# Performance work log

Hardware: AMD Instinct MI355X
Metric: run time of the kernel (lower is better)

## Reference

```python
import jax, jax.numpy as jnp
import numpy as np

N_FILTERS = 1024
N_HEADS = 16


def setup_inputs() -> dict:
    key = jax.random.key(0)
    k1, k2, k3 = jax.random.split(key, 3)
    x = jax.random.normal(k1, (8, 1024, N_FILTERS), dtype=jnp.float32)
    # VarianceScaling(0.02) ~ small dense init; 0.02*sqrt(1/fan_in) scale approximated
    w_qkv = jax.random.normal(k2, (N_FILTERS, N_FILTERS * 3), dtype=jnp.float32) * (0.02 / N_FILTERS) ** 0.5
    w_out = jax.random.normal(k3, (N_FILTERS, N_FILTERS), dtype=jnp.float32) * (0.02 / N_FILTERS) ** 0.5
    return {"x": x, "w_qkv": w_qkv, "w_out": w_out}


def reference(x, w_qkv, w_out):
    b, n, c = x.shape
    h = N_HEADS
    d = c // h
    qkv = jnp.einsum('bnc,ce->bne', x, w_qkv)  # [b, n, 3c]
    q, k, v = jnp.split(qkv, 3, axis=-1)
    # b n (h d) -> b h n d
    to_heads = lambda t: t.reshape(b, n, h, d).transpose(0, 2, 1, 3)
    q, k, v = to_heads(q), to_heads(k), to_heads(v)
    scale = jnp.sqrt(jnp.asarray(c, jnp.float32))  # NOTE: sqrt(n_filters), matches source
    attn = jnp.einsum('bhnd,bhmd->bhnm', q, k) / scale
    attn = jax.nn.softmax(attn, axis=-1)
    out = jnp.einsum('bhnm,bhmd->bhnd', attn, v)
    out = out.transpose(0, 2, 1, 3).reshape(b, n, c)  # b h n d -> b n (h d)
    return jnp.einsum('bnc,co->bno', out, w_out)
```

## Files before the change

### kernel.cpp

```cpp
#include <hip/hip_runtime.h>
#include <hip/hip_bf16.h>

typedef __bf16 bf16_t;
typedef __bf16 bf16x8 __attribute__((ext_vector_type(8)));
typedef __bf16 bf16x4 __attribute__((ext_vector_type(4)));
typedef float f32x4 __attribute__((ext_vector_type(4)));

constexpr int LD = 3072;

#define MFMA_16x16x32(a, b, c) __builtin_amdgcn_mfma_f32_16x16x32_bf16((a), (b), (c), 0, 0, 0)

#define GLOAD_LDS16(g, l)                                               \
  __builtin_amdgcn_global_load_lds(                                     \
      (const __attribute__((address_space(1))) void*)(g),               \
      (__attribute__((address_space(3))) void*)(l), 16, 0, 0)

#define TRREAD(dst, addr, imm) \
  asm volatile("ds_read_b64_tr_b16 %0, %1 offset:" imm : "=v"(dst) : "v"(addr))

#define BAR __builtin_amdgcn_s_barrier()
#define LGKM0 do { asm volatile("s_waitcnt lgkmcnt(0)" ::: "memory"); \
                   __builtin_amdgcn_sched_barrier(0); } while (0)

__global__ __launch_bounds__(256) void prep_kernel(
    const float* __restrict__ x, bf16_t* __restrict__ x_b,
    const float* __restrict__ w_qkv, bf16_t* __restrict__ wqT,
    const float* __restrict__ w_out, bf16_t* __restrict__ woT) {
  const int blk = blockIdx.x;
  if (blk < 4096) {
    const int i = blk * 256 + threadIdx.x;
    const float4 a = reinterpret_cast<const float4*>(x)[2 * i];
    const float4 c = reinterpret_cast<const float4*>(x)[2 * i + 1];
    bf16x8 o;
    o[0] = (bf16_t)a.x; o[1] = (bf16_t)a.y; o[2] = (bf16_t)a.z; o[3] = (bf16_t)a.w;
    o[4] = (bf16_t)c.x; o[5] = (bf16_t)c.y; o[6] = (bf16_t)c.z; o[7] = (bf16_t)c.w;
    reinterpret_cast<bf16x8*>(x_b)[i] = o;
    return;
  }
  __shared__ float tile[32][33];
  const float* in; bf16_t* outp; int C, bx, by;
  if (blk < 7168) { const int i = blk - 4096; in = w_qkv; outp = wqT; C = 3072; bx = i % 96; by = i / 96; }
  else            { const int i = blk - 7168; in = w_out; outp = woT; C = 1024; bx = i & 31; by = i >> 5; }
  constexpr int R = 1024;
  const int c0 = bx * 32, r0 = by * 32;
  const int tx = threadIdx.x & 31, ty = threadIdx.x >> 5;
#pragma unroll
  for (int i = 0; i < 32; i += 8)
    tile[ty + i][tx] = in[(size_t)(r0 + ty + i) * C + (c0 + tx)];
  __syncthreads();
#pragma unroll
  for (int i = 0; i < 32; i += 8)
    outp[(size_t)(c0 + ty + i) * R + (r0 + tx)] = (bf16_t)tile[tx][ty + i];
}

__global__ __launch_bounds__(512, 2) void gemm_qkv_256(
    const bf16_t* __restrict__ A, const bf16_t* __restrict__ Bt,
    bf16_t* __restrict__ C, float q_scale) {
  constexpr int K = 1024;
  extern __shared__ char smem[];
  char* asB = smem;
  char* bsB = smem + 65536;

  const int t = threadIdx.x;
  const int lane = t & 63, wave = t >> 6;
  const int l15 = lane & 15, lg = lane >> 4;
  const int wr = wave >> 2, wc = wave & 3;

  const int bid = blockIdx.x;
  const int wg = (bid & 7) * 48 + (bid >> 3);
  const int brow = (wg & 31) * 256;
  const int bcol = (wg >> 5) * 256;

  const int srow = t >> 3;
  const int schk = (t & 7) ^ (srow & 7);
  const bf16_t* aS = A + (size_t)(brow + srow) * K + schk * 8;
  const bf16_t* bS = Bt + (size_t)(bcol + srow) * K + schk * 8;
  const int ldst = t * 8;

#define STG_A(T, H) do {                                                      \
    const bf16_t* _s = aS + (size_t)((H) * 128) * K + (T) * 64;               \
    bf16_t* _d = (bf16_t*)(asB + ((T) & 1) * 32768 + (H) * 16384) + ldst;     \
    GLOAD_LDS16(_s, _d);                                                      \
    GLOAD_LDS16(_s + (size_t)64 * K, _d + 4096);                              \
  } while (0)
#define STG_B(T, H) do {                                                      \
    const bf16_t* _s = bS + (size_t)((H) * 128) * K + (T) * 64;               \
    bf16_t* _d = (bf16_t*)(bsB + ((T) & 1) * 32768 + (H) * 16384) + ldst;     \
    GLOAD_LDS16(_s, _d);                                                      \
    GLOAD_LDS16(_s + (size_t)64 * K, _d + 4096);                              \
  } while (0)

  const int rx = l15 & 7;
  const unsigned c0 = ((unsigned)(lg ^ rx)) << 4;
  const unsigned c1 = ((unsigned)((4 | lg) ^ rx)) << 4;
  const unsigned a_rd = (unsigned)(wr * 16384 + l15 * 128);
  const unsigned b_rd = (unsigned)((wc >> 1) * 16384 + (wc & 1) * 8192 + l15 * 128);

  f32x4 acc[8][4] = {};
  bf16x8 af[4][2], bfr[2][2];

#define RD_AF(BUF, MH) do { _Pragma("unroll")                                 \
    for (int m = 0; m < 4; ++m) {                                             \
      const char* _p = asB + (BUF) * 32768 + a_rd + ((MH) * 4 + m) * 2048;    \
      af[m][0] = *(const bf16x8*)(_p + c0);                                   \
      af[m][1] = *(const bf16x8*)(_p + c1); } } while (0)
#define RD_BF(BUF, NH) do { _Pragma("unroll")                                 \
    for (int n = 0; n < 2; ++n) {                                             \
      const char* _p = bsB + (BUF) * 32768 + b_rd + ((NH) * 2 + n) * 2048;    \
      bfr[n][0] = *(const bf16x8*)(_p + c0);                                  \
      bfr[n][1] = *(const bf16x8*)(_p + c1); } } while (0)
#define MM16(MH, NH) do {                                                     \
    __builtin_amdgcn_s_setprio(1);                                            \
    _Pragma("unroll")                                                         \
    for (int m = 0; m < 4; ++m) { _Pragma("unroll")                           \
      for (int n = 0; n < 2; ++n) {                                           \
        acc[(MH)*4+m][(NH)*2+n] =                                             \
            MFMA_16x16x32(af[m][0], bfr[n][0], acc[(MH)*4+m][(NH)*2+n]);      \
        acc[(MH)*4+m][(NH)*2+n] =                                             \
            MFMA_16x16x32(af[m][1], bfr[n][1], acc[(MH)*4+m][(NH)*2+n]); } }  \
    __builtin_amdgcn_s_setprio(0); } while (0)

  STG_A(0, 0); STG_A(0, 1); STG_B(0, 0); STG_B(0, 1); STG_A(1, 0);
  asm volatile("s_waitcnt vmcnt(2)" ::: "memory");
  BAR;

  for (int i = 0; i < 8; ++i) {
    const int T1 = 2 * i + 1, T2 = 2 * i + 2, T3 = 2 * i + 3;
    const bool pf = (i < 7);
    STG_A(T1, 1);
    RD_AF(0, 0); RD_BF(0, 0);
    BAR; LGKM0; MM16(0, 0); BAR;
    STG_B(T1, 0);
    RD_BF(0, 1);
    BAR; LGKM0; MM16(0, 1); BAR;
    STG_B(T1, 1);
    RD_AF(0, 1);
    BAR; LGKM0; MM16(1, 1); BAR;
    if (pf) STG_A(T2, 0);
    RD_BF(0, 0);
    BAR; LGKM0; MM16(1, 0);
    if (pf) asm volatile("s_waitcnt vmcnt(2)" ::: "memory");
    else    asm volatile("s_waitcnt vmcnt(0)" ::: "memory");
    BAR;
    if (pf) STG_A(T2, 1);
    RD_AF(1, 0); RD_BF(1, 0);
    BAR; LGKM0; MM16(0, 0); BAR;
    if (pf) STG_B(T2, 0);
    RD_BF(1, 1);
    BAR; LGKM0; MM16(0, 1); BAR;
    if (pf) STG_B(T2, 1);
    RD_AF(1, 1);
    BAR; LGKM0; MM16(1, 1); BAR;
    if (pf) STG_A(T3, 0);
    RD_BF(1, 0);
    BAR; LGKM0; MM16(1, 0);
    asm volatile("s_waitcnt vmcnt(2)" ::: "memory");
    BAR;
  }

  const float sc = (bcol < 1024) ? q_scale : 1.0f;
  const int crow0 = brow + wr * 128 + lg * 4;
  const int ccol0 = bcol + wc * 64 + l15;
#pragma unroll
  for (int m = 0; m < 8; ++m)
#pragma unroll
    for (int n = 0; n < 4; ++n)
#pragma unroll
      for (int r = 0; r < 4; ++r)
        C[(size_t)(crow0 + m * 16 + r) * 3072 + ccol0 + n * 16] =
            (bf16_t)(acc[m][n][r] * sc);
#undef STG_A
#undef STG_B
#undef RD_AF
#undef RD_BF
#undef MM16
}

template <typename OutT>
__global__ __launch_bounds__(512, 1) void gemm_bt_128x256(
    const bf16_t* __restrict__ A, const bf16_t* __restrict__ Bt,
    OutT* __restrict__ C, int N, int nrowblk, int q_cols, float q_scale) {
  constexpr int K = 1024;
  extern __shared__ char smem[];
  char* asB = smem;
  char* bsB = smem + 49152;

  const int t = threadIdx.x;
  const int lane = t & 63, wave = t >> 6;
  const int l15 = lane & 15, lg = lane >> 4;
  const int wr = wave >> 2, wc = wave & 3;

  const int cpx = (int)gridDim.x >> 3;
  const int bid = blockIdx.x;
  const int wg = (bid & 7) * cpx + (bid >> 3);
  const int brow = (wg % nrowblk) * 128;
  const int bcol = (wg / nrowblk) * 256;

  const int srow = t >> 3;
  const int schk = (t & 7) ^ (srow & 7);
  const bf16_t* aS = A + (size_t)(brow + srow) * K + schk * 8;
  const bf16_t* bS = Bt + (size_t)(bcol + srow) * K + schk * 8;
  const int ldst = t * 8;

#define STG_A(T, BUF) do {                                               \
    const bf16_t* _s = aS + (T) * 64;                                    \
    bf16_t* _d = (bf16_t*)(asB + (BUF) * 16384) + ldst;                  \
    GLOAD_LDS16(_s, _d);                                                 \
    GLOAD_LDS16(_s + (size_t)64 * K, _d + 4096);                         \
  } while (0)
#define STG_B(T, H, BUF) do {                                            \
    const bf16_t* _s = bS + (size_t)((H) * 128) * K + (T) * 64;          \
    bf16_t* _d = (bf16_t*)(bsB + (BUF) * 32768 + (H) * 16384) + ldst;    \
    GLOAD_LDS16(_s, _d);                                                 \
    GLOAD_LDS16(_s + (size_t)64 * K, _d + 4096);                         \
  } while (0)

  const int rx = l15 & 7;
  const unsigned c0 = ((unsigned)(lg ^ rx)) << 4;
  const unsigned c1 = ((unsigned)((4 | lg) ^ rx)) << 4;
  const unsigned a_rd = (unsigned)(wr * 8192 + l15 * 128);
  const unsigned b_rd = (unsigned)((wc >> 1) * 16384 + (wc & 1) * 8192 + l15 * 128);

  f32x4 acc[4][4] = {};
  bf16x8 af[2][2], bfr[4][2];

#define RD_AF(BUF, MH) do { _Pragma("unroll")                            \
    for (int m = 0; m < 2; ++m) {                                        \
      const char* _p = asB + (BUF) * 16384 + a_rd + ((MH) * 2 + m) * 2048; \
      af[m][0] = *(const bf16x8*)(_p + c0);                              \
      af[m][1] = *(const bf16x8*)(_p + c1); } } while (0)
#define RD_BF(BUF) do { _Pragma("unroll")                                \
    for (int n = 0; n < 4; ++n) {                                        \
      const char* _p = bsB + (BUF) * 32768 + b_rd + n * 2048;            \
      bfr[n][0] = *(const bf16x8*)(_p + c0);                             \
      bfr[n][1] = *(const bf16x8*)(_p + c1); } } while (0)
#define MM(MH) do {                                                      \
    __builtin_amdgcn_s_setprio(1);                                       \
    _Pragma("unroll")                                                    \
    for (int m = 0; m < 2; ++m) { _Pragma("unroll")                      \
      for (int n = 0; n < 4; ++n) {                                      \
        acc[(MH)*2+m][n] =                                               \
            MFMA_16x16x32(af[m][0], bfr[n][0], acc[(MH)*2+m][n]);        \
        acc[(MH)*2+m][n] =                                               \
            MFMA_16x16x32(af[m][1], bfr[n][1], acc[(MH)*2+m][n]); } }    \
    __builtin_amdgcn_s_setprio(0); } while (0)

  STG_A(0, 0); STG_B(0, 0, 0); STG_B(0, 1, 0);
  STG_A(1, 1); STG_B(1, 0, 1); STG_B(1, 1, 1);
  asm volatile("s_waitcnt vmcnt(6)" ::: "memory");
  BAR;

  int bc = 0;
  for (int T = 0; T < 16; ++T) {
    const bool pf = (T + 2 < 16);
    const int bs = (bc >= 1) ? (bc - 1) : 2;
    if (pf) { STG_A(T + 2, bs); STG_B(T + 2, 0, bs); }
    RD_AF(bc, 0);
    RD_BF(bc);
    BAR; LGKM0; MM(0); BAR;
    if (pf) STG_B(T + 2, 1, bs);
    RD_AF(bc, 1);
    BAR; LGKM0; MM(1);
    if (pf) asm volatile("s_waitcnt vmcnt(6)" ::: "memory");
    else    asm volatile("s_waitcnt vmcnt(0)" ::: "memory");
    BAR;
    bc = (bc == 2) ? 0 : bc + 1;
  }

  const float sc = (bcol < q_cols) ? q_scale : 1.0f;
  const int crow0 = brow + wr * 64 + lg * 4;
  const int ccol0 = bcol + wc * 64 + l15;
#pragma unroll
  for (int m = 0; m < 4; ++m)
#pragma unroll
    for (int n = 0; n < 4; ++n)
#pragma unroll
      for (int r = 0; r < 4; ++r)
        C[(size_t)(crow0 + m * 16 + r) * N + ccol0 + n * 16] =
            (OutT)(acc[m][n][r] * sc);
#undef STG_A
#undef STG_B
#undef RD_AF
#undef RD_BF
#undef MM
}

__device__ __forceinline__ unsigned pack_bf16_pair(float a, float b) {
  union { __hip_bfloat162 h; unsigned u; } c;
  c.h = __float22bfloat162_rn(float2{a, b});
  return c.u;
}

__global__ __launch_bounds__(256, 3) void attn_kernel(const bf16_t* __restrict__ qkv,
                                                      bf16_t* __restrict__ ctx) {
  __shared__ bf16_t Ks[3][4096];
  __shared__ bf16_t Vs[3][4096];
  const int tid = threadIdx.x, lane = tid & 63, wave = tid >> 6;
  const int l15 = lane & 15, lg = (lane >> 4) & 3;
  const int flat = blockIdx.x;
  const int xcd = flat & 7, rr = flat >> 3;
  const int qt = rr & 7;
  const int hb = xcd * 16 + (rr >> 3);
  const int h = hb & 15, b = hb >> 4;
  const size_t base = (size_t)b * 1024 * LD;
  const int qbase = qt * 128 + wave * 32;

  bf16x8 qa[2][2];
#pragma unroll
  for (int s = 0; s < 2; s++) {
    const bf16_t* qp = qkv + base + (size_t)(qbase + s * 16 + l15) * LD + h * 64 + lg * 8;
    qa[s][0] = *reinterpret_cast<const bf16x8*>(qp);
    qa[s][1] = *reinterpret_cast<const bf16x8*>(qp + 32);
  }

  const bf16_t* Kb = qkv + base + 1024 + h * 64;
  const bf16_t* Vb = qkv + base + 2048 + h * 64;

  const int krr = lane >> 3;
  const int kcc = (lane & 7) ^ krr;
  const bf16_t* ksrc0 = Kb + (size_t)(wave * 16 + krr) * LD + kcc * 8;
  const bf16_t* ksrc1 = ksrc0 + (size_t)8 * LD;

  const int vd0 = (lane & 1) * 8 + wave * 16;
  const int vkv = ((lane >> 1) & 3) + ((lane >> 3) & 3) * 4 + (lane >> 5) * 16;
  const bf16_t* vsrc0 = Vb + (size_t)vkv * LD + vd0;
  const bf16_t* vsrc1 = vsrc0 + (size_t)32 * LD;

  bf16_t* ksb = &Ks[0][0];
  bf16_t* vsb = &Vs[0][0];
  const char* ksr = (const char*)&Ks[0][0];
  const unsigned vs_byte =
      (unsigned)(size_t)(__attribute__((address_space(3))) void*)(&Vs[0][0]);
  const unsigned tr_lane = vs_byte + lane * 8;

  const int rx7 = l15 & 7;
  const unsigned kb0 = (unsigned)(l15 * 128 + ((lg ^ rx7) << 4));
  const unsigned kb1 = (unsigned)(l15 * 128 + (((4 | lg) ^ rx7) << 4));

  bf16x8 ones;
#pragma unroll
  for (int j = 0; j < 8; j++) ones[j] = (bf16_t)1.0f;

  f32x4 dn[2] = {};
  f32x4 oacc[2][4] = {};

#define STAGE(BUF, T) do {                                               \
    const size_t _go = (size_t)(T) * 64 * LD;                            \
    bf16_t* _kd = ksb + (BUF) * 4096 + wave * 1024;                      \
    bf16_t* _vd = vsb + (BUF) * 4096 + wave * 1024;                      \
    GLOAD_LDS16(ksrc0 + _go, _kd);                                       \
    GLOAD_LDS16(ksrc1 + _go, _kd + 512);                                 \
    GLOAD_LDS16(vsrc0 + _go, _vd);                                       \
    GLOAD_LDS16(vsrc1 + _go, _vd + 512);                                 \
  } while (0)

  STAGE(0, 0);
  STAGE(1, 1);
  asm volatile("s_waitcnt vmcnt(4)" ::: "memory");
  __builtin_amdgcn_sched_barrier(0);
  BAR;

  int bc = 0;
  for (int t = 0; t < 16; t++) {
    const int bsg = (bc == 0) ? 2 : bc - 1;
    if (t < 14) STAGE(bsg, t + 2);

    f32x4 sacc[2][4] = {};
    const char* kt = ksr + bc * 8192;
    __builtin_amdgcn_s_setprio(1);
#pragma unroll
    for (int tt = 0; tt < 4; tt++) {
      const bf16x8 k0 = *reinterpret_cast<const bf16x8*>(kt + tt * 2048 + kb0);
      const bf16x8 k1 = *reinterpret_cast<const bf16x8*>(kt + tt * 2048 + kb1);
      sacc[0][tt] = MFMA_16x16x32(k0, qa[0][0], sacc[0][tt]);
      sacc[0][tt] = MFMA_16x16x32(k1, qa[0][1], sacc[0][tt]);
      sacc[1][tt] = MFMA_16x16x32(k0, qa[1][0], sacc[1][tt]);
      sacc[1][tt] = MFMA_16x16x32(k1, qa[1][1], sacc[1][tt]);
    }
    __builtin_amdgcn_s_setprio(0);

    const unsigned ta = tr_lane + (unsigned)(bc * 8192);
    bf16x4 tl0, th0, tl2, th2, tl4, th4, tl6, th6;
    TRREAD(tl0, ta, "0");    TRREAD(th0, ta, "512");
    TRREAD(tl2, ta, "2048"); TRREAD(th2, ta, "2560");
    TRREAD(tl4, ta, "4096"); TRREAD(th4, ta, "4608");
    TRREAD(tl6, ta, "6144"); TRREAD(th6, ta, "6656");
    __builtin_amdgcn_sched_barrier(0);

    unsigned pu[16];
#pragma unroll
    for (int tt = 0; tt < 4; tt++) {
      const float a0 = __builtin_exp2f(sacc[0][tt][0]);
      const float a1 = __builtin_exp2f(sacc[0][tt][1]);
      const float a2 = __builtin_exp2f(sacc[0][tt][2]);
      const float a3 = __builtin_exp2f(sacc[0][tt][3]);
      pu[(tt >> 1) * 4 + (tt & 1) * 2 + 0] = pack_bf16_pair(a0, a1);
      pu[(tt >> 1) * 4 + (tt & 1) * 2 + 1] = pack_bf16_pair(a2, a3);
      const float b0 = __builtin_exp2f(sacc[1][tt][0]);
      const float b1 = __builtin_exp2f(sacc[1][tt][1]);
      const float b2 = __builtin_exp2f(sacc[1][tt][2]);
      const float b3 = __builtin_exp2f(sacc[1][tt][3]);
      pu[8 + (tt >> 1) * 4 + (tt & 1) * 2 + 0] = pack_bf16_pair(b0, b1);
      pu[8 + (tt >> 1) * 4 + (tt & 1) * 2 + 1] = pack_bf16_pair(b2, b3);
    }
    bf16x8 pa[2][2];
    pa[0][0] = *reinterpret_cast<bf16x8*>(&pu[0]);
    pa[0][1] = *reinterpret_cast<bf16x8*>(&pu[4]);
    pa[1][0] = *reinterpret_cast<bf16x8*>(&pu[8]);
    pa[1][1] = *reinterpret_cast<bf16x8*>(&pu[12]);

    dn[0] = MFMA_16x16x32(pa[0][0], ones, dn[0]);
    dn[0] = MFMA_16x16x32(pa[0][1], ones, dn[0]);
    dn[1] = MFMA_16x16x32(pa[1][0], ones, dn[1]);
    dn[1] = MFMA_16x16x32(pa[1][1], ones, dn[1]);

    bf16x4 tl1, th1, tl3, th3, tl5, th5, tl7, th7;
    TRREAD(tl1, ta, "1024"); TRREAD(th1, ta, "1536");
    TRREAD(tl3, ta, "3072"); TRREAD(th3, ta, "3584");
    TRREAD(tl5, ta, "5120"); TRREAD(th5, ta, "5632");
    TRREAD(tl7, ta, "7168"); TRREAD(th7, ta, "7680");

    asm volatile("s_waitcnt lgkmcnt(8)" ::: "memory");
    __builtin_amdgcn_sched_barrier(0);
    {
      bf16x8 vb0[4];
      vb0[0] = __builtin_shufflevector(tl0, th0, 0, 1, 2, 3, 4, 5, 6, 7);
      vb0[1] = __builtin_shufflevector(tl2, th2, 0, 1, 2, 3, 4, 5, 6, 7);
      vb0[2] = __builtin_shufflevector(tl4, th4, 0, 1, 2, 3, 4, 5, 6, 7);
      vb0[3] = __builtin_shufflevector(tl6, th6, 0, 1, 2, 3, 4, 5, 6, 7);
      __builtin_amdgcn_s_setprio(1);
#pragma unroll
      for (int s = 0; s < 2; s++)
#pragma unroll
        for (int dt = 0; dt < 4; dt++)
          oacc[s][dt] = MFMA_16x16x32(pa[s][0], vb0[dt], oacc[s][dt]);
      __builtin_amdgcn_s_setprio(0);
    }

    asm volatile("s_waitcnt lgkmcnt(0)" ::: "memory");
    __builtin_amdgcn_sched_barrier(0);
    {
      bf16x8 vb1[4];
      vb1[0] = __builtin_shufflevector(tl1, th1, 0, 1, 2, 3, 4, 5, 6, 7);
      vb1[1] = __builtin_shufflevector(tl3, th3, 0, 1, 2, 3, 4, 5, 6, 7);
      vb1[2] = __builtin_shufflevector(tl5, th5, 0, 1, 2, 3, 4, 5, 6, 7);
      vb1[3] = __builtin_shufflevector(tl7, th7, 0, 1, 2, 3, 4, 5, 6, 7);
      __builtin_amdgcn_s_setprio(1);
#pragma unroll
      for (int s = 0; s < 2; s++)
#pragma unroll
        for (int dt = 0; dt < 4; dt++)
          oacc[s][dt] = MFMA_16x16x32(pa[s][1], vb1[dt], oacc[s][dt]);
      __builtin_amdgcn_s_setprio(0);
    }

    if (t < 14) asm volatile("s_waitcnt vmcnt(4)" ::: "memory");
    else        asm volatile("s_waitcnt vmcnt(0)" ::: "memory");
    __builtin_amdgcn_sched_barrier(0);
    BAR;

    bc = (bc == 2) ? 0 : bc + 1;
  }

#pragma unroll
  for (int s = 0; s < 2; s++) {
#pragma unroll
    for (int r = 0; r < 4; r++) {
      const float inv = 1.0f / dn[s][r];
      const size_t row = (size_t)(b * 1024 + qbase + s * 16 + lg * 4 + r);
#pragma unroll
      for (int dt = 0; dt < 4; dt++)
        ctx[row * 1024 + h * 64 + dt * 16 + l15] = (bf16_t)(oacc[s][dt][r] * inv);
    }
  }
#undef STAGE
}

extern "C" void kernel_launch(void* const* d_in, const int* in_sizes, int n_in,
                              void* d_out, int out_size, void* d_ws, size_t ws_size,
                              hipStream_t stream) {
  (void)in_sizes; (void)n_in; (void)out_size; (void)ws_size;
  const float* x = (const float*)d_in[0];
  const float* w_qkv = (const float*)d_in[1];
  const float* w_out = (const float*)d_in[2];
  float* out = (float*)d_out;
  char* ws = (char*)d_ws;

  bf16_t* x_b   = (bf16_t*)(ws);
  bf16_t* qkv_b = (bf16_t*)(ws + (size_t)(16 << 20));
  bf16_t* wqT   = (bf16_t*)(ws + (size_t)(64 << 20));
  bf16_t* woT   = (bf16_t*)(ws + (size_t)(70 << 20));
  bf16_t* ctx_b = (bf16_t*)(ws + (size_t)(72 << 20));

  const float qsc = 0.045084220027780106f;

  prep_kernel<<<8192, 256, 0, stream>>>(x, x_b, w_qkv, wqT, w_out, woT);
  gemm_qkv_256<<<384, 512, 131072, stream>>>(x_b, wqT, qkv_b, qsc);
  attn_kernel<<<1024, 256, 0, stream>>>(qkv_b, ctx_b);
  gemm_bt_128x256<float><<<256, 512, 147456, stream>>>(
      ctx_b, woT, out, 1024, 64, 0, 1.0f);
}
```

Before: 161.1 us.

## Shrink QKV GEMM K-tile to 32 with static LDS and higher occupancy

Restructures the QKV projection GEMM so each K step covers 32 elements instead of 64. The dynamic 128KB LDS allocation becomes a static 64KB double buffer, and the swizzle and fragment reads are rewritten to match. Launch bounds go from 2 to 4 blocks per CU. The aim is more resident blocks to hide latency, at the cost of four times as many barrier and wait cycles over the K loop, and register pressure may limit the extra occupancy.

After: 444.1 us. 2.76x slower.

```diff
diff --git a/kernel.cpp b/kernel.cpp
--- a/kernel.cpp
+++ b/kernel.cpp
@@ -53,13 +53,12 @@
     outp[(size_t)(c0 + ty + i) * R + (r0 + tx)] = (bf16_t)tile[tx][ty + i];
 }
 
-__global__ __launch_bounds__(512, 2) void gemm_qkv_256(
+__global__ __launch_bounds__(512, 4) void gemm_qkv_256(
     const bf16_t* __restrict__ A, const bf16_t* __restrict__ Bt,
     bf16_t* __restrict__ C, float q_scale) {
   constexpr int K = 1024;
-  extern __shared__ char smem[];
-  char* asB = smem;
-  char* bsB = smem + 65536;
+  __shared__ char asB[2][16384];
+  __shared__ char bsB[2][16384];
 
   const int t = threadIdx.x;
   const int lane = t & 63, wave = t >> 6;
@@ -71,90 +70,65 @@
   const int brow = (wg & 31) * 256;
   const int bcol = (wg >> 5) * 256;
 
-  const int srow = t >> 3;
-  const int schk = (t & 7) ^ (srow & 7);
+  const int srow = t >> 2;
+  const int schk = (t & 3) ^ ((t >> 3) & 3);
   const bf16_t* aS = A + (size_t)(brow + srow) * K + schk * 8;
   const bf16_t* bS = Bt + (size_t)(bcol + srow) * K + schk * 8;
   const int ldst = t * 8;
 
-#define STG_A(T, H) do {                                                      \
-    const bf16_t* _s = aS + (size_t)((H) * 128) * K + (T) * 64;               \
-    bf16_t* _d = (bf16_t*)(asB + ((T) & 1) * 32768 + (H) * 16384) + ldst;     \
-    GLOAD_LDS16(_s, _d);                                                      \
-    GLOAD_LDS16(_s + (size_t)64 * K, _d + 4096);                              \
-  } while (0)
-#define STG_B(T, H) do {                                                      \
-    const bf16_t* _s = bS + (size_t)((H) * 128) * K + (T) * 64;               \
-    bf16_t* _d = (bf16_t*)(bsB + ((T) & 1) * 32768 + (H) * 16384) + ldst;     \
-    GLOAD_LDS16(_s, _d);                                                      \
-    GLOAD_LDS16(_s + (size_t)64 * K, _d + 4096);                              \
-  } while (0)
-
-  const int rx = l15 & 7;
-  const unsigned c0 = ((unsigned)(lg ^ rx)) << 4;
-  const unsigned c1 = ((unsigned)((4 | lg) ^ rx)) << 4;
-  const unsigned a_rd = (unsigned)(wr * 16384 + l15 * 128);
-  const unsigned b_rd = (unsigned)((wc >> 1) * 16384 + (wc & 1) * 8192 + l15 * 128);
+#define STG_A(T, BUF) do {                                               \
+    const bf16_t* _s = aS + (T) * 32;                                    \
+    bf16_t* _d = (bf16_t*)(&asB[BUF][0]) + ldst;                         \
+    GLOAD_LDS16(_s, _d);                                                 \
+    GLOAD_LDS16(_s + (size_t)128 * K, _d + 4096);                        \
+  } while (0)
+#define STG_B(T, BUF) do {                                               \
+    const bf16_t* _s = bS + (T) * 32;                                    \
+    bf16_t* _d = (bf16_t*)(&bsB[BUF][0]) + ldst;                         \
+    GLOAD_LDS16(_s, _d);                                                 \
+    GLOAD_LDS16(_s + (size_t)128 * K, _d + 4096);                        \
+  } while (0)
+
+  const unsigned cX = ((unsigned)(lg ^ ((l15 >> 1) & 3))) << 4;
+  const unsigned a_rd = (unsigned)((wr * 128 + l15) * 64) + cX;
+  const unsigned b_rd = (unsigned)((wc * 64 + l15) * 64) + cX;
 
   f32x4 acc[8][4] = {};
-  bf16x8 af[4][2], bfr[2][2];
-
-#define RD_AF(BUF, MH) do { _Pragma("unroll")                                 \
-    for (int m = 0; m < 4; ++m) {                                             \
-      const char* _p = asB + (BUF) * 32768 + a_rd + ((MH) * 4 + m) * 2048;    \
-      af[m][0] = *(const bf16x8*)(_p + c0);                                   \
-      af[m][1] = *(const bf16x8*)(_p + c1); } } while (0)
-#define RD_BF(BUF, NH) do { _Pragma("unroll")                                 \
-    for (int n = 0; n < 2; ++n) {                                             \
-      const char* _p = bsB + (BUF) * 32768 + b_rd + ((NH) * 2 + n) * 2048;    \
-      bfr[n][0] = *(const bf16x8*)(_p + c0);                                  \
-      bfr[n][1] = *(const bf16x8*)(_p + c1); } } while (0)
-#define MM16(MH, NH) do {                                                     \
-    __builtin_amdgcn_s_setprio(1);                                            \
-    _Pragma("unroll")                                                         \
-    for (int m = 0; m < 4; ++m) { _Pragma("unroll")                           \
-      for (int n = 0; n < 2; ++n) {                                           \
-        acc[(MH)*4+m][(NH)*2+n] =                                             \
-            MFMA_16x16x32(af[m][0], bfr[n][0], acc[(MH)*4+m][(NH)*2+n]);      \
-        acc[(MH)*4+m][(NH)*2+n] =                                             \
-            MFMA_16x16x32(af[m][1], bfr[n][1], acc[(MH)*4+m][(NH)*2+n]); } }  \
+  bf16x8 af[4], bfr[4];
+
+#define RD_AF(BUF, MH) do { _Pragma("unroll")                            \
+    for (int m = 0; m < 4; ++m)                                          \
+      af[m] = *(const bf16x8*)(&asB[BUF][0] + a_rd + (MH) * 4096 + m * 1024); \
+  } while (0)
+#define RD_BF(BUF) do { _Pragma("unroll")                                \
+    for (int n = 0; n < 4; ++n)                                          \
+      bfr[n] = *(const bf16x8*)(&bsB[BUF][0] + b_rd + n * 1024);         \
+  } while (0)
+#define MM(MH) do {                                                      \
+    __builtin_amdgcn_s_setprio(1);                                       \
+    _Pragma("unroll")                                                    \
+    for (int m = 0; m < 4; ++m) { _Pragma("unroll")                      \
+      for (int n = 0; n < 4; ++n)                                        \
+        acc[(MH)*4+m][n] = MFMA_16x16x32(af[m], bfr[n], acc[(MH)*4+m][n]); } \
     __builtin_amdgcn_s_setprio(0); } while (0)
 
-  STG_A(0, 0); STG_A(0, 1); STG_B(0, 0); STG_B(0, 1); STG_A(1, 0);
-  asm volatile("s_waitcnt vmcnt(2)" ::: "memory");
+  STG_A(0, 0); STG_B(0, 0);
+  asm volatile("s_waitcnt vmcnt(0)" ::: "memory");
+  __builtin_amdgcn_sched_barrier(0);
   BAR;
 
-  for (int i = 0; i < 8; ++i) {
-    const int T1 = 2 * i + 1, T2 = 2 * i + 2, T3 = 2 * i + 3;
-    const bool pf = (i < 7);
-    STG_A(T1, 1);
-    RD_AF(0, 0); RD_BF(0, 0);
-    BAR; LGKM0; MM16(0, 0); BAR;
-    STG_B(T1, 0);
-    RD_BF(0, 1);
-    BAR; LGKM0; MM16(0, 1); BAR;
-    STG_B(T1, 1);
-    RD_AF(0, 1);
-    BAR; LGKM0; MM16(1, 1); BAR;
-    if (pf) STG_A(T2, 0);
-    RD_BF(0, 0);
-    BAR; LGKM0; MM16(1, 0);
-    if (pf) asm volatile("s_waitcnt vmcnt(2)" ::: "memory");
-    else    asm volatile("s_waitcnt vmcnt(0)" ::: "memory");
-    BAR;
-    if (pf) STG_A(T2, 1);
-    RD_AF(1, 0); RD_BF(1, 0);
-    BAR; LGKM0; MM16(0, 0); BAR;
-    if (pf) STG_B(T2, 0);
-    RD_BF(1, 1);
-    BAR; LGKM0; MM16(0, 1); BAR;
-    if (pf) STG_B(T2, 1);
-    RD_AF(1, 1);
-    BAR; LGKM0; MM16(1, 1); BAR;
-    if (pf) STG_A(T3, 0);
-    RD_BF(1, 0);
-    BAR; LGKM0; MM16(1, 0);
-    asm volatile("s_waitcnt vmcnt(2)" ::: "memory");
+  for (int T = 0; T < 32; ++T) {
+    const int bc = T & 1;
+    const bool pf = (T < 31);
+    if (pf) STG_A(T + 1, bc ^ 1);
+    RD_BF(bc);
+    RD_AF(bc, 0);
+    BAR; LGKM0; MM(0); BAR;
+    if (pf) STG_B(T + 1, bc ^ 1);
+    RD_AF(bc, 1);
+    BAR; LGKM0; MM(1);
+    asm volatile("s_waitcnt vmcnt(0)" ::: "memory");
+    __builtin_amdgcn_sched_barrier(0);
     BAR;
   }
 
@@ -173,7 +147,7 @@
 #undef STG_B
 #undef RD_AF
 #undef RD_BF
-#undef MM16
+#undef MM
 }
 
 template <typename OutT>
@@ -495,7 +469,7 @@
   const float qsc = 0.045084220027780106f;
 
   prep_kernel<<<8192, 256, 0, stream>>>(x, x_b, w_qkv, wqT, w_out, woT);
-  gemm_qkv_256<<<384, 512, 131072, stream>>>(x_b, wqT, qkv_b, qsc);
+  gemm_qkv_256<<<384, 512, 0, stream>>>(x_b, wqT, qkv_b, qsc);
   attn_kernel<<<1024, 256, 0, stream>>>(qkv_b, ctx_b);
   gemm_bt_128x256<float><<<256, 512, 147456, stream>>>(
       ctx_b, woT, out, 1024, 64, 0, 1.0f);
```
